# Kernel tuning notes

Hardware: AMD Instinct MI355X
Metric: run time of the kernel (lower is better)

## Reference

```python
import jax, jax.numpy as jnp
import numpy as np

B, I, H, D, PF, K = 256, 1024, 8, 128, 2, 4
P = PF * I          # up-projection width
HD = H * D          # hidden dim
EPS = 1e-5


def setup_inputs() -> dict:
    key = jax.random.key(0)
    ks = jax.random.split(key, 16)
    g = lambda k, shape, s=0.02: (jax.random.normal(k, shape, jnp.float32) * s)
    return dict(
        seq=jax.random.normal(ks[0], (B, I), jnp.float32),
        c0=jnp.zeros((B, H, D, D), jnp.float32),
        n0=jnp.ones((B, H, D), jnp.float32),
        m0=jnp.zeros((B, H), jnp.float32),
        ln_g=jnp.ones((I,), jnp.float32), ln_b=jnp.zeros((I,), jnp.float32),
        gn_g=jnp.ones((HD,), jnp.float32), gn_b=jnp.zeros((HD,), jnp.float32),
        W_upl=g(ks[1], (P, I)), b_upl=jnp.zeros((P,), jnp.float32),
        W_upr=g(ks[2], (HD, I)), b_upr=jnp.zeros((HD,), jnp.float32),
        W_down=g(ks[3], (I, HD)), b_down=jnp.zeros((I,), jnp.float32),
        conv_w=g(ks[4], (K,), 0.3), conv_b=jnp.zeros((1,), jnp.float32),
        W_skip=g(ks[5], (HD, P)),
        W_i=g(ks[6], (H, P)), b_i=jnp.zeros((H,), jnp.float32),
        W_f=g(ks[7], (H, P)), b_f=jnp.zeros((H,), jnp.float32),
        W_o=g(ks[8], (HD, P)), b_o=jnp.zeros((HD,), jnp.float32),
        W_q=g(ks[9], (HD, P)), b_q=jnp.zeros((HD,), jnp.float32),
        W_k=g(ks[10], (HD, P)), b_k=jnp.zeros((HD,), jnp.float32),
        W_v=g(ks[11], (HD, P)), b_v=jnp.zeros((HD,), jnp.float32),
    )


def reference(seq, c0, n0, m0, ln_g, ln_b, gn_g, gn_b,
              W_upl, b_upl, W_upr, b_upr, W_down, b_down,
              conv_w, conv_b, W_skip,
              W_i, b_i, W_f, b_f, W_o, b_o,
              W_q, b_q, W_k, b_k, W_v, b_v):
    # LayerNorm on input
    mu = seq.mean(-1, keepdims=True)
    var = seq.var(-1, keepdims=True)
    x_n = (seq - mu) / jnp.sqrt(var + EPS) * ln_g + ln_b

    x_t = x_n @ W_upl.T + b_upl      # [B, P]
    r_t = x_n @ W_upr.T + b_upr      # [B, HD]

    # Causal conv (kernel K) along the feature axis of x_t
    xp = jnp.pad(x_t, ((0, 0), (K - 1, 0)))
    x_c = sum(conv_w[j] * xp[:, j:j + P] for j in range(K)) + conv_b[0]
    x_c = jax.nn.silu(x_c)           # [B, P]

    q = (x_c @ W_q.T + b_q).reshape(B, H, D)
    k = (x_c @ W_k.T + b_k).reshape(B, H, D) / np.float32(np.sqrt(D))
    v = (x_t @ W_v.T + b_v).reshape(B, H, D)

    i_t = x_c @ W_i.T + b_i          # [B, H]
    f_t = x_c @ W_f.T + b_f          # [B, H]
    o_t = jax.nn.sigmoid(x_t @ W_o.T + b_o)  # [B, HD]

    # Stabilized exponential gating
    m_t = jnp.maximum(f_t + m0, i_t)
    i_e = jnp.exp(i_t - m_t)
    f_e = jnp.exp(f_t - m_t + m0)

    # Matrix-memory covariance update: f*C + i*(v x k)
    c_t = f_e[:, :, None, None] * c0 + i_e[:, :, None, None] * jnp.einsum('bhd,bhp->bhdp', v, k)
    n_t = f_e[:, :, None] * n0 + i_e[:, :, None] * k

    num = jnp.einsum('bhdp,bhp->bhd', c_t, q)
    den = jnp.clip(jnp.einsum('bhd,bhd->bh', n_t, q), 1.0, None)[..., None]
    h_t = o_t * (num / den).reshape(B, HD)

    # GroupNorm: H groups of D channels, per-channel affine
    hg = h_t.reshape(B, H, D)
    gmu = hg.mean(-1, keepdims=True)
    gvar = hg.var(-1, keepdims=True)
    h_norm = ((hg - gmu) / jnp.sqrt(gvar + EPS)).reshape(B, HD) * gn_g + gn_b

    out = h_norm + x_c @ W_skip.T    # skip: 1x1 conv == linear, no bias
    out = out * jax.nn.silu(r_t)
    out = out @ W_down.T + b_down
    return (out + seq, c_t, n_t, m_t)
```

## Files before the change

kernel.cpp:

```cpp
#include <hip/hip_runtime.h>
#include <hip/hip_bf16.h>

typedef __attribute__((ext_vector_type(8))) short short8;
typedef __attribute__((ext_vector_type(4))) float f32x4;

__device__ __forceinline__ unsigned short f2bf(float x) {
  union { float f; unsigned int u; } v; v.f = x;
  unsigned int r = v.u + 0x7FFFu + ((v.u >> 16) & 1u);
  return (unsigned short)(r >> 16);
}

__global__ __launch_bounds__(256) void ln_kernel(
    const float* __restrict__ seq, const float* __restrict__ g,
    const float* __restrict__ b, unsigned short* __restrict__ xnb) {
  int row = blockIdx.x;
  int tid = threadIdx.x;
  const float* x = seq + (size_t)row * 1024;
  float4 v = *(const float4*)(x + tid * 4);
  float s = v.x + v.y + v.z + v.w;
  float s2 = v.x * v.x + v.y * v.y + v.z * v.z + v.w * v.w;
#pragma unroll
  for (int off = 32; off; off >>= 1) { s += __shfl_down(s, off); s2 += __shfl_down(s2, off); }
  __shared__ float rs_[4], rs2_[4];
  int lane = tid & 63, wave = tid >> 6;
  if (lane == 0) { rs_[wave] = s; rs2_[wave] = s2; }
  __syncthreads();
  float sum = rs_[0] + rs_[1] + rs_[2] + rs_[3];
  float sum2 = rs2_[0] + rs2_[1] + rs2_[2] + rs2_[3];
  float mu = sum * (1.f / 1024.f);
  float var = sum2 * (1.f / 1024.f) - mu * mu;
  float rstd = rsqrtf(var + 1e-5f);
  float4 gg = *(const float4*)(g + tid * 4);
  float4 bb = *(const float4*)(b + tid * 4);
  ushort4 o;
  o.x = f2bf((v.x - mu) * rstd * gg.x + bb.x);
  o.y = f2bf((v.y - mu) * rstd * gg.y + bb.y);
  o.z = f2bf((v.z - mu) * rstd * gg.z + bb.z);
  o.w = f2bf((v.w - mu) * rstd * gg.w + bb.w);
  *(ushort4*)(xnb + (size_t)row * 1024 + tid * 4) = o;
}

struct GemmSegs {
  const unsigned short* A[8];
  const float* W[8];
  const float* bias[8];
  const float* add[8];
  float* out[8];
  int N[8];
  int tile0[8];
  int act[8];
  float scale[8];
  int nseg;
  int K;
};

#define SB 72

__global__ __launch_bounds__(256, 4) void gemm_multi(GemmSegs g) {
  __shared__ __align__(16) unsigned short As[64 * SB];
  __shared__ __align__(16) unsigned short Ws[64 * SB];
  int bid = blockIdx.x;
  int m0 = (bid & 3) * 64;
  int tIdx = bid >> 2;
  int s = 0;
  while (s + 1 < g.nseg && tIdx >= g.tile0[s + 1]) s++;
  int n0 = (tIdx - g.tile0[s]) * 64;
  const unsigned short* A = g.A[s];
  const float* W = g.W[s];
  int N = g.N[s], Kd = g.K;
  int tid = threadIdx.x;
  int lane = tid & 63, wave = tid >> 6, quad = lane >> 4, l16 = lane & 15;

  f32x4 acc[4] = {};

  int r_ = tid >> 2;
  int c_ = (tid & 3) * 16;

  const unsigned short* aRow = A + (size_t)(m0 + r_) * Kd + c_;
  const float* wRow = W + (size_t)(n0 + r_) * Kd + c_;
  bool wOk = (n0 + r_) < N;

  uint4 a0 = *(const uint4*)(aRow);
  uint4 a1 = *(const uint4*)(aRow + 8);
  float4 w0 = make_float4(0, 0, 0, 0), w1 = w0, w2 = w0, w3 = w0;
  if (wOk) {
    w0 = *(const float4*)(wRow);
    w1 = *(const float4*)(wRow + 4);
    w2 = *(const float4*)(wRow + 8);
    w3 = *(const float4*)(wRow + 12);
  }

  for (int k0 = 0; k0 < Kd; k0 += 64) {
    *(uint4*)&As[r_ * SB + c_] = a0;
    *(uint4*)&As[r_ * SB + c_ + 8] = a1;
    uint4 u0, u1;
    u0.x = (unsigned)f2bf(w0.x) | ((unsigned)f2bf(w0.y) << 16);
    u0.y = (unsigned)f2bf(w0.z) | ((unsigned)f2bf(w0.w) << 16);
    u0.z = (unsigned)f2bf(w1.x) | ((unsigned)f2bf(w1.y) << 16);
    u0.w = (unsigned)f2bf(w1.z) | ((unsigned)f2bf(w1.w) << 16);
    u1.x = (unsigned)f2bf(w2.x) | ((unsigned)f2bf(w2.y) << 16);
    u1.y = (unsigned)f2bf(w2.z) | ((unsigned)f2bf(w2.w) << 16);
    u1.z = (unsigned)f2bf(w3.x) | ((unsigned)f2bf(w3.y) << 16);
    u1.w = (unsigned)f2bf(w3.z) | ((unsigned)f2bf(w3.w) << 16);
    *(uint4*)&Ws[r_ * SB + c_] = u0;
    *(uint4*)&Ws[r_ * SB + c_ + 8] = u1;
    __syncthreads();
    if (k0 + 64 < Kd) {
      a0 = *(const uint4*)(aRow + k0 + 64);
      a1 = *(const uint4*)(aRow + k0 + 72);
      if (wOk) {
        w0 = *(const float4*)(wRow + k0 + 64);
        w1 = *(const float4*)(wRow + k0 + 68);
        w2 = *(const float4*)(wRow + k0 + 72);
        w3 = *(const float4*)(wRow + k0 + 76);
      }
    }
#pragma unroll
    for (int kc = 0; kc < 2; kc++) {
      int kb = kc * 32 + quad * 8;
      short8 af = *(const short8*)&As[(wave * 16 + l16) * SB + kb];
#pragma unroll
      for (int c = 0; c < 4; c++) {
        short8 bfr = *(const short8*)&Ws[(c * 16 + l16) * SB + kb];
        acc[c] = __builtin_amdgcn_mfma_f32_16x16x32_bf16(af, bfr, acc[c], 0, 0, 0);
      }
    }
    __syncthreads();
  }

  const float* bias = g.bias[s];
  const float* add = g.add[s];
  float* out = g.out[s];
  int act = g.act[s];
  float scale = g.scale[s];
#pragma unroll
  for (int c = 0; c < 4; c++) {
    int n = n0 + c * 16 + l16;
    if (n >= N) continue;
    float bv = bias ? bias[n] : 0.f;
#pragma unroll
    for (int j = 0; j < 4; j++) {
      int m = m0 + wave * 16 + quad * 4 + j;
      float val = acc[c][j] + bv;
      if (act == 1) val = val / (1.f + __expf(-val));
      else if (act == 2) val = 1.f / (1.f + __expf(-val));
      val *= scale;
      size_t idx = (size_t)m * N + n;
      if (act == 3) val += add[idx];
      out[idx] = val;
    }
  }
}

__global__ __launch_bounds__(256) void conv_kernel(
    const float* __restrict__ xt, const float* __restrict__ conv_w,
    const float* __restrict__ conv_b, unsigned short* __restrict__ xcb,
    unsigned short* __restrict__ xtb) {
  int b = blockIdx.x;
  int tid = threadIdx.x;
  __shared__ float xr[2048];
  const float* row = xt + (size_t)b * 2048;
#pragma unroll
  for (int it = 0; it < 2; it++) {
    int i = (it * 256 + tid) * 4;
    *(float4*)&xr[i] = *(const float4*)(row + i);
  }
  __syncthreads();
  float w0 = conv_w[0], w1 = conv_w[1], w2 = conv_w[2], w3 = conv_w[3], cb = conv_b[0];
#pragma unroll
  for (int it = 0; it < 2; it++) {
    int i0 = (it * 256 + tid) * 4;
    ushort4 oc, ot;
    unsigned short* pc = &oc.x;
    unsigned short* pt = &ot.x;
#pragma unroll
    for (int j = 0; j < 4; j++) {
      int i = i0 + j;
      float x3 = xr[i];
      float x2 = (i >= 1) ? xr[i - 1] : 0.f;
      float x1 = (i >= 2) ? xr[i - 2] : 0.f;
      float x0 = (i >= 3) ? xr[i - 3] : 0.f;
      float c = w0 * x0 + w1 * x1 + w2 * x2 + w3 * x3 + cb;
      c = c / (1.f + __expf(-c));
      pc[j] = f2bf(c);
      pt[j] = f2bf(x3);
    }
    *(ushort4*)(xcb + (size_t)b * 2048 + i0) = oc;
    *(ushort4*)(xtb + (size_t)b * 2048 + i0) = ot;
  }
}

__global__ __launch_bounds__(256) void cell_kernel(
    const float* __restrict__ c0, const float* __restrict__ n0,
    const float* __restrict__ m0, const float* __restrict__ qb,
    const float* __restrict__ kb, const float* __restrict__ vb,
    const float* __restrict__ ob, const float* __restrict__ skipb,
    const float* __restrict__ srb, const float* __restrict__ itb,
    const float* __restrict__ ftb, const float* __restrict__ gn_g,
    const float* __restrict__ gn_b, float* __restrict__ ct_out,
    float* __restrict__ nt_out, float* __restrict__ mt_out,
    unsigned short* __restrict__ yb) {
  int bh = blockIdx.x;
  int h = bh & 7;
  int tid = threadIdx.x;
  int lane = tid & 63, wave = tid >> 6;
  __shared__ float qs[128], ks[128], vs[128], num[128];
  __shared__ float r0[4], r1[4];

  float i_t = itb[bh], f_t = ftb[bh], m0v = m0[bh];
  float m_t = fmaxf(f_t + m0v, i_t);
  float i_e = __expf(i_t - m_t);
  float f_e = __expf(f_t - m_t + m0v);
  if (tid == 0) mt_out[bh] = m_t;

  size_t vbase = (size_t)bh * 128;
  float kq_p = 0.f, nq_p = 0.f, n0d = 0.f, kd = 0.f;
  if (tid < 128) {
    float qd = qb[vbase + tid];
    kd = kb[vbase + tid];
    n0d = n0[vbase + tid];
    qs[tid] = qd; ks[tid] = kd; vs[tid] = vb[vbase + tid];
    kq_p = kd * qd;
    nq_p = n0d * qd;
  }
#pragma unroll
  for (int off = 32; off; off >>= 1) { kq_p += __shfl_down(kq_p, off); nq_p += __shfl_down(nq_p, off); }
  if (lane == 0) { r0[wave] = kq_p; r1[wave] = nq_p; }
  __syncthreads();
  float kq = r0[0] + r0[1] + r0[2] + r0[3];
  float nq = r1[0] + r1[1] + r1[2] + r1[3];
  float den = fmaxf(f_e * nq + i_e * kq, 1.f);

  if (tid < 128) nt_out[vbase + tid] = f_e * n0d + i_e * kd;

  int rsub = lane >> 3;
  int cblk = lane & 7;
  int ccol = cblk * 16;
  float kr[16], qr[16];
#pragma unroll
  for (int j = 0; j < 16; j += 4) {
    *(float4*)&kr[j] = *(const float4*)&ks[ccol + j];
    *(float4*)&qr[j] = *(const float4*)&qs[ccol + j];
  }
  const float* c0p = c0 + (size_t)bh * 16384;
  float* ctp = ct_out + (size_t)bh * 16384;
#pragma unroll
  for (int gI = 0; gI < 4; gI++) {
    int d = wave * 32 + gI * 8 + rsub;
    float iv = i_e * vs[d];
    const float* src = c0p + d * 128 + ccol;
    float* dst = ctp + d * 128 + ccol;
    float p = 0.f;
#pragma unroll
    for (int j = 0; j < 4; j++) {
      float4 cv = *(const float4*)(src + j * 4);
      float4 cn;
      cn.x = f_e * cv.x + iv * kr[j * 4 + 0];
      cn.y = f_e * cv.y + iv * kr[j * 4 + 1];
      cn.z = f_e * cv.z + iv * kr[j * 4 + 2];
      cn.w = f_e * cv.w + iv * kr[j * 4 + 3];
      *(float4*)(dst + j * 4) = cn;
      p += cn.x * qr[j * 4 + 0] + cn.y * qr[j * 4 + 1] +
           cn.z * qr[j * 4 + 2] + cn.w * qr[j * 4 + 3];
    }
    p += __shfl_xor(p, 1);
    p += __shfl_xor(p, 2);
    p += __shfl_xor(p, 4);
    if (cblk == 0) num[d] = p;
  }
  __syncthreads();

  float hval = 0.f;
  if (tid < 128) hval = ob[vbase + tid] * num[tid] / den;
  float s = hval, s2 = hval * hval;
#pragma unroll
  for (int off = 32; off; off >>= 1) { s += __shfl_down(s, off); s2 += __shfl_down(s2, off); }
  if (lane == 0) { r0[wave] = s; r1[wave] = s2; }
  __syncthreads();
  float mean = (r0[0] + r0[1] + r0[2] + r0[3]) * (1.f / 128.f);
  float var = (r1[0] + r1[1] + r1[2] + r1[3]) * (1.f / 128.f) - mean * mean;
  float rstd = rsqrtf(var + 1e-5f);
  if (tid < 128) {
    int ch = h * 128 + tid;
    float hn = (hval - mean) * rstd * gn_g[ch] + gn_b[ch];
    float y = (hn + skipb[vbase + tid]) * srb[vbase + tid];
    yb[vbase + tid] = f2bf(y);
  }
}

extern "C" void kernel_launch(void* const* d_in, const int* in_sizes, int n_in,
                              void* d_out, int out_size, void* d_ws, size_t ws_size,
                              hipStream_t stream) {
  const float* seq   = (const float*)d_in[0];
  const float* c0    = (const float*)d_in[1];
  const float* n0    = (const float*)d_in[2];
  const float* m0    = (const float*)d_in[3];
  const float* ln_g  = (const float*)d_in[4];
  const float* ln_b  = (const float*)d_in[5];
  const float* gn_g  = (const float*)d_in[6];
  const float* gn_b  = (const float*)d_in[7];
  const float* W_upl = (const float*)d_in[8];
  const float* b_upl = (const float*)d_in[9];
  const float* W_upr = (const float*)d_in[10];
  const float* b_upr = (const float*)d_in[11];
  const float* W_down= (const float*)d_in[12];
  const float* b_down= (const float*)d_in[13];
  const float* conv_w= (const float*)d_in[14];
  const float* conv_b= (const float*)d_in[15];
  const float* W_skip= (const float*)d_in[16];
  const float* W_i   = (const float*)d_in[17];
  const float* b_i   = (const float*)d_in[18];
  const float* W_f   = (const float*)d_in[19];
  const float* b_f   = (const float*)d_in[20];
  const float* W_o   = (const float*)d_in[21];
  const float* b_o   = (const float*)d_in[22];
  const float* W_q   = (const float*)d_in[23];
  const float* b_q   = (const float*)d_in[24];
  const float* W_k   = (const float*)d_in[25];
  const float* b_k   = (const float*)d_in[26];
  const float* W_v   = (const float*)d_in[27];
  const float* b_v   = (const float*)d_in[28];

  float* out = (float*)d_out;
  float* ct  = out + 262144;
  float* nt  = ct + 33554432;
  float* mt  = nt + 262144;

  char* ws = (char*)d_ws;
  unsigned short* xnb = (unsigned short*)(ws);
  unsigned short* xtb = (unsigned short*)(ws + 524288);
  unsigned short* xcb = (unsigned short*)(ws + 1572864);
  unsigned short* yb  = (unsigned short*)(ws + 2621440);
  float* xt  = (float*)(ws + 3145728);
  float* sr  = (float*)(ws + 5242880);
  float* qb  = (float*)(ws + 6291456);
  float* kb  = (float*)(ws + 7340032);
  float* vb  = (float*)(ws + 8388608);
  float* ob  = (float*)(ws + 9437184);
  float* skb = (float*)(ws + 10485760);
  float* itb = (float*)(ws + 11534336);
  float* ftb = (float*)(ws + 11542528);

  ln_kernel<<<256, 256, 0, stream>>>(seq, ln_g, ln_b, xnb);

  GemmSegs g1 = {};
  g1.nseg = 2; g1.K = 1024;
  g1.A[0] = xnb; g1.W[0] = W_upl; g1.bias[0] = b_upl; g1.out[0] = xt;
  g1.N[0] = 2048; g1.tile0[0] = 0;  g1.act[0] = 0; g1.scale[0] = 1.f;
  g1.A[1] = xnb; g1.W[1] = W_upr; g1.bias[1] = b_upr; g1.out[1] = sr;
  g1.N[1] = 1024; g1.tile0[1] = 32; g1.act[1] = 1; g1.scale[1] = 1.f;
  gemm_multi<<<48 * 4, 256, 0, stream>>>(g1);

  conv_kernel<<<256, 256, 0, stream>>>(xt, conv_w, conv_b, xcb, xtb);

  GemmSegs g2 = {};
  g2.nseg = 7; g2.K = 2048;
  g2.A[0] = xcb; g2.W[0] = W_q;    g2.bias[0] = b_q;    g2.out[0] = qb;
  g2.N[0] = 1024; g2.tile0[0] = 0;  g2.act[0] = 0; g2.scale[0] = 1.f;
  g2.A[1] = xcb; g2.W[1] = W_k;    g2.bias[1] = b_k;    g2.out[1] = kb;
  g2.N[1] = 1024; g2.tile0[1] = 16; g2.act[1] = 0; g2.scale[1] = 0.088388347648318447f;
  g2.A[2] = xtb; g2.W[2] = W_v;    g2.bias[2] = b_v;    g2.out[2] = vb;
  g2.N[2] = 1024; g2.tile0[2] = 32; g2.act[2] = 0; g2.scale[2] = 1.f;
  g2.A[3] = xtb; g2.W[3] = W_o;    g2.bias[3] = b_o;    g2.out[3] = ob;
  g2.N[3] = 1024; g2.tile0[3] = 48; g2.act[3] = 2; g2.scale[3] = 1.f;
  g2.A[4] = xcb; g2.W[4] = W_skip; g2.bias[4] = nullptr; g2.out[4] = skb;
  g2.N[4] = 1024; g2.tile0[4] = 64; g2.act[4] = 0; g2.scale[4] = 1.f;
  g2.A[5] = xcb; g2.W[5] = W_i;    g2.bias[5] = b_i;    g2.out[5] = itb;
  g2.N[5] = 8;    g2.tile0[5] = 80; g2.act[5] = 0; g2.scale[5] = 1.f;
  g2.A[6] = xcb; g2.W[6] = W_f;    g2.bias[6] = b_f;    g2.out[6] = ftb;
  g2.N[6] = 8;    g2.tile0[6] = 81; g2.act[6] = 0; g2.scale[6] = 1.f;
  gemm_multi<<<82 * 4, 256, 0, stream>>>(g2);

  cell_kernel<<<2048, 256, 0, stream>>>(c0, n0, m0, qb, kb, vb, ob, skb, sr,
                                        itb, ftb, gn_g, gn_b, ct, nt, mt, yb);

  GemmSegs g3 = {};
  g3.nseg = 1; g3.K = 1024;
  g3.A[0] = yb; g3.W[0] = W_down; g3.bias[0] = b_down; g3.add[0] = seq; g3.out[0] = out;
  g3.N[0] = 1024; g3.tile0[0] = 0; g3.act[0] = 3; g3.scale[0] = 1.f;
  gemm_multi<<<16 * 4, 256, 0, stream>>>(g3);
}
```

Before: 419.1 us.

## Pre-convert weights to bf16 in a prep kernel and coalesce cell C-update

A new prep_kernel converts all fp32 weight matrices to bf16 once per call into workspace. The GEMMs then load bf16 weights directly, removing the per-tile fp32 load and bf16 conversion that was repeated across the four M-blocks. This adds an extra launch and a full pass over the weights (fp32 read, bf16 write). Separately, the cell kernel's C-state update now has 32 lanes cover each 128-float row with float4 accesses over 16 passes, for more coalesced memory traffic, at the cost of a longer shuffle reduction per row.

```diff
diff --git a/kernel.cpp b/kernel.cpp
--- a/kernel.cpp
+++ b/kernel.cpp
@@ -8,6 +8,35 @@
   union { float f; unsigned int u; } v; v.f = x;
   unsigned int r = v.u + 0x7FFFu + ((v.u >> 16) & 1u);
   return (unsigned short)(r >> 16);
+}
+
+struct PrepSegs {
+  const float* src[10];
+  unsigned short* dst[10];
+  int blk0[10];
+  int nseg;
+};
+
+__global__ __launch_bounds__(256) void prep_kernel(PrepSegs p) {
+  int bid = blockIdx.x;
+  int s = 0;
+  while (s + 1 < p.nseg && bid >= p.blk0[s + 1]) s++;
+  size_t off = (size_t)(bid - p.blk0[s]) * 8192;
+  const float* src = p.src[s] + off;
+  unsigned short* dst = p.dst[s] + off;
+  int tid = threadIdx.x;
+#pragma unroll
+  for (int j = 0; j < 4; j++) {
+    int i = (j * 256 + tid) * 8;
+    float4 a = *(const float4*)(src + i);
+    float4 b = *(const float4*)(src + i + 4);
+    uint4 o;
+    o.x = (unsigned)f2bf(a.x) | ((unsigned)f2bf(a.y) << 16);
+    o.y = (unsigned)f2bf(a.z) | ((unsigned)f2bf(a.w) << 16);
+    o.z = (unsigned)f2bf(b.x) | ((unsigned)f2bf(b.y) << 16);
+    o.w = (unsigned)f2bf(b.z) | ((unsigned)f2bf(b.w) << 16);
+    *(uint4*)(dst + i) = o;
+  }
 }
 
 __global__ __launch_bounds__(256) void ln_kernel(
@@ -42,7 +71,7 @@
 
 struct GemmSegs {
   const unsigned short* A[8];
-  const float* W[8];
+  const unsigned short* W[8];
   const float* bias[8];
   const float* add[8];
   float* out[8];
@@ -66,7 +95,7 @@
   while (s + 1 < g.nseg && tIdx >= g.tile0[s + 1]) s++;
   int n0 = (tIdx - g.tile0[s]) * 64;
   const unsigned short* A = g.A[s];
-  const float* W = g.W[s];
+  const unsigned short* W = g.W[s];
   int N = g.N[s], Kd = g.K;
   int tid = threadIdx.x;
   int lane = tid & 63, wave = tid >> 6, quad = lane >> 4, l16 = lane & 15;
@@ -77,42 +106,30 @@
   int c_ = (tid & 3) * 16;
 
   const unsigned short* aRow = A + (size_t)(m0 + r_) * Kd + c_;
-  const float* wRow = W + (size_t)(n0 + r_) * Kd + c_;
+  const unsigned short* wRow = W + (size_t)(n0 + r_) * Kd + c_;
   bool wOk = (n0 + r_) < N;
 
+  uint4 zz = make_uint4(0, 0, 0, 0);
   uint4 a0 = *(const uint4*)(aRow);
   uint4 a1 = *(const uint4*)(aRow + 8);
-  float4 w0 = make_float4(0, 0, 0, 0), w1 = w0, w2 = w0, w3 = w0;
+  uint4 w0 = zz, w1 = zz;
   if (wOk) {
-    w0 = *(const float4*)(wRow);
-    w1 = *(const float4*)(wRow + 4);
-    w2 = *(const float4*)(wRow + 8);
-    w3 = *(const float4*)(wRow + 12);
+    w0 = *(const uint4*)(wRow);
+    w1 = *(const uint4*)(wRow + 8);
   }
 
   for (int k0 = 0; k0 < Kd; k0 += 64) {
     *(uint4*)&As[r_ * SB + c_] = a0;
     *(uint4*)&As[r_ * SB + c_ + 8] = a1;
-    uint4 u0, u1;
-    u0.x = (unsigned)f2bf(w0.x) | ((unsigned)f2bf(w0.y) << 16);
-    u0.y = (unsigned)f2bf(w0.z) | ((unsigned)f2bf(w0.w) << 16);
-    u0.z = (unsigned)f2bf(w1.x) | ((unsigned)f2bf(w1.y) << 16);
-    u0.w = (unsigned)f2bf(w1.z) | ((unsigned)f2bf(w1.w) << 16);
-    u1.x = (unsigned)f2bf(w2.x) | ((unsigned)f2bf(w2.y) << 16);
-    u1.y = (unsigned)f2bf(w2.z) | ((unsigned)f2bf(w2.w) << 16);
-    u1.z = (unsigned)f2bf(w3.x) | ((unsigned)f2bf(w3.y) << 16);
-    u1.w = (unsigned)f2bf(w3.z) | ((unsigned)f2bf(w3.w) << 16);
-    *(uint4*)&Ws[r_ * SB + c_] = u0;
-    *(uint4*)&Ws[r_ * SB + c_ + 8] = u1;
+    *(uint4*)&Ws[r_ * SB + c_] = w0;
+    *(uint4*)&Ws[r_ * SB + c_ + 8] = w1;
     __syncthreads();
     if (k0 + 64 < Kd) {
       a0 = *(const uint4*)(aRow + k0 + 64);
       a1 = *(const uint4*)(aRow + k0 + 72);
       if (wOk) {
-        w0 = *(const float4*)(wRow + k0 + 64);
-        w1 = *(const float4*)(wRow + k0 + 68);
-        w2 = *(const float4*)(wRow + k0 + 72);
-        w3 = *(const float4*)(wRow + k0 + 76);
+        w0 = *(const uint4*)(wRow + k0 + 64);
+        w1 = *(const uint4*)(wRow + k0 + 72);
       }
     }
 #pragma unroll
@@ -233,40 +250,30 @@
 
   if (tid < 128) nt_out[vbase + tid] = f_e * n0d + i_e * kd;
 
-  int rsub = lane >> 3;
-  int cblk = lane & 7;
-  int ccol = cblk * 16;
-  float kr[16], qr[16];
-#pragma unroll
-  for (int j = 0; j < 16; j += 4) {
-    *(float4*)&kr[j] = *(const float4*)&ks[ccol + j];
-    *(float4*)&qr[j] = *(const float4*)&qs[ccol + j];
-  }
+  int col = (tid & 31) * 4;
+  int drow = tid >> 5;
+  float4 kr = *(const float4*)&ks[col];
+  float4 qr = *(const float4*)&qs[col];
   const float* c0p = c0 + (size_t)bh * 16384;
   float* ctp = ct_out + (size_t)bh * 16384;
-#pragma unroll
-  for (int gI = 0; gI < 4; gI++) {
-    int d = wave * 32 + gI * 8 + rsub;
+#pragma unroll 4
+  for (int pass = 0; pass < 16; pass++) {
+    int d = pass * 8 + drow;
     float iv = i_e * vs[d];
-    const float* src = c0p + d * 128 + ccol;
-    float* dst = ctp + d * 128 + ccol;
-    float p = 0.f;
-#pragma unroll
-    for (int j = 0; j < 4; j++) {
-      float4 cv = *(const float4*)(src + j * 4);
-      float4 cn;
-      cn.x = f_e * cv.x + iv * kr[j * 4 + 0];
-      cn.y = f_e * cv.y + iv * kr[j * 4 + 1];
-      cn.z = f_e * cv.z + iv * kr[j * 4 + 2];
-      cn.w = f_e * cv.w + iv * kr[j * 4 + 3];
-      *(float4*)(dst + j * 4) = cn;
-      p += cn.x * qr[j * 4 + 0] + cn.y * qr[j * 4 + 1] +
-           cn.z * qr[j * 4 + 2] + cn.w * qr[j * 4 + 3];
-    }
+    float4 cv = *(const float4*)(c0p + d * 128 + col);
+    float4 cn;
+    cn.x = f_e * cv.x + iv * kr.x;
+    cn.y = f_e * cv.y + iv * kr.y;
+    cn.z = f_e * cv.z + iv * kr.z;
+    cn.w = f_e * cv.w + iv * kr.w;
+    *(float4*)(ctp + d * 128 + col) = cn;
+    float p = cn.x * qr.x + cn.y * qr.y + cn.z * qr.z + cn.w * qr.w;
     p += __shfl_xor(p, 1);
     p += __shfl_xor(p, 2);
     p += __shfl_xor(p, 4);
-    if (cblk == 0) num[d] = p;
+    p += __shfl_xor(p, 8);
+    p += __shfl_xor(p, 16);
+    if ((tid & 31) == 0) num[d] = p;
   }
   __syncthreads();
 
@@ -340,14 +347,39 @@
   float* skb = (float*)(ws + 10485760);
   float* itb = (float*)(ws + 11534336);
   float* ftb = (float*)(ws + 11542528);
+  unsigned short* wb = (unsigned short*)(ws + 11550720);
+  unsigned short* wupl_b = wb;
+  unsigned short* wupr_b = wupl_b + 2097152;
+  unsigned short* wdown_b= wupr_b + 1048576;
+  unsigned short* wskip_b= wdown_b + 1048576;
+  unsigned short* wq_b   = wskip_b + 2097152;
+  unsigned short* wk_b   = wq_b + 2097152;
+  unsigned short* wv_b   = wk_b + 2097152;
+  unsigned short* wo_b   = wv_b + 2097152;
+  unsigned short* wi_b   = wo_b + 2097152;
+  unsigned short* wf_b   = wi_b + 16384;
+
+  PrepSegs pp = {};
+  pp.nseg = 10;
+  pp.src[0] = W_upl;  pp.dst[0] = wupl_b;  pp.blk0[0] = 0;
+  pp.src[1] = W_upr;  pp.dst[1] = wupr_b;  pp.blk0[1] = 256;
+  pp.src[2] = W_down; pp.dst[2] = wdown_b; pp.blk0[2] = 384;
+  pp.src[3] = W_skip; pp.dst[3] = wskip_b; pp.blk0[3] = 512;
+  pp.src[4] = W_q;    pp.dst[4] = wq_b;    pp.blk0[4] = 768;
+  pp.src[5] = W_k;    pp.dst[5] = wk_b;    pp.blk0[5] = 1024;
+  pp.src[6] = W_v;    pp.dst[6] = wv_b;    pp.blk0[6] = 1280;
+  pp.src[7] = W_o;    pp.dst[7] = wo_b;    pp.blk0[7] = 1536;
+  pp.src[8] = W_i;    pp.dst[8] = wi_b;    pp.blk0[8] = 1792;
+  pp.src[9] = W_f;    pp.dst[9] = wf_b;    pp.blk0[9] = 1794;
+  prep_kernel<<<1796, 256, 0, stream>>>(pp);
 
   ln_kernel<<<256, 256, 0, stream>>>(seq, ln_g, ln_b, xnb);
 
   GemmSegs g1 = {};
   g1.nseg = 2; g1.K = 1024;
-  g1.A[0] = xnb; g1.W[0] = W_upl; g1.bias[0] = b_upl; g1.out[0] = xt;
+  g1.A[0] = xnb; g1.W[0] = wupl_b; g1.bias[0] = b_upl; g1.out[0] = xt;
   g1.N[0] = 2048; g1.tile0[0] = 0;  g1.act[0] = 0; g1.scale[0] = 1.f;
-  g1.A[1] = xnb; g1.W[1] = W_upr; g1.bias[1] = b_upr; g1.out[1] = sr;
+  g1.A[1] = xnb; g1.W[1] = wupr_b; g1.bias[1] = b_upr; g1.out[1] = sr;
   g1.N[1] = 1024; g1.tile0[1] = 32; g1.act[1] = 1; g1.scale[1] = 1.f;
   gemm_multi<<<48 * 4, 256, 0, stream>>>(g1);
 
@@ -355,19 +387,19 @@
 
   GemmSegs g2 = {};
   g2.nseg = 7; g2.K = 2048;
-  g2.A[0] = xcb; g2.W[0] = W_q;    g2.bias[0] = b_q;    g2.out[0] = qb;
+  g2.A[0] = xcb; g2.W[0] = wq_b;    g2.bias[0] = b_q;    g2.out[0] = qb;
   g2.N[0] = 1024; g2.tile0[0] = 0;  g2.act[0] = 0; g2.scale[0] = 1.f;
-  g2.A[1] = xcb; g2.W[1] = W_k;    g2.bias[1] = b_k;    g2.out[1] = kb;
+  g2.A[1] = xcb; g2.W[1] = wk_b;    g2.bias[1] = b_k;    g2.out[1] = kb;
   g2.N[1] = 1024; g2.tile0[1] = 16; g2.act[1] = 0; g2.scale[1] = 0.088388347648318447f;
-  g2.A[2] = xtb; g2.W[2] = W_v;    g2.bias[2] = b_v;    g2.out[2] = vb;
+  g2.A[2] = xtb; g2.W[2] = wv_b;    g2.bias[2] = b_v;    g2.out[2] = vb;
   g2.N[2] = 1024; g2.tile0[2] = 32; g2.act[2] = 0; g2.scale[2] = 1.f;
-  g2.A[3] = xtb; g2.W[3] = W_o;    g2.bias[3] = b_o;    g2.out[3] = ob;
+  g2.A[3] = xtb; g2.W[3] = wo_b;    g2.bias[3] = b_o;    g2.out[3] = ob;
   g2.N[3] = 1024; g2.tile0[3] = 48; g2.act[3] = 2; g2.scale[3] = 1.f;
-  g2.A[4] = xcb; g2.W[4] = W_skip; g2.bias[4] = nullptr; g2.out[4] = skb;
+  g2.A[4] = xcb; g2.W[4] = wskip_b; g2.bias[4] = nullptr; g2.out[4] = skb;
   g2.N[4] = 1024; g2.tile0[4] = 64; g2.act[4] = 0; g2.scale[4] = 1.f;
-  g2.A[5] = xcb; g2.W[5] = W_i;    g2.bias[5] = b_i;    g2.out[5] = itb;
+  g2.A[5] = xcb; g2.W[5] = wi_b;    g2.bias[5] = b_i;    g2.out[5] = itb;
   g2.N[5] = 8;    g2.tile0[5] = 80; g2.act[5] = 0; g2.scale[5] = 1.f;
-  g2.A[6] = xcb; g2.W[6] = W_f;    g2.bias[6] = b_f;    g2.out[6] = ftb;
+  g2.A[6] = xcb; g2.W[6] = wf_b;    g2.bias[6] = b_f;    g2.out[6] = ftb;
   g2.N[6] = 8;    g2.tile0[6] = 81; g2.act[6] = 0; g2.scale[6] = 1.f;
   gemm_multi<<<82 * 4, 256, 0, stream>>>(g2);
 
@@ -376,7 +408,7 @@
 
   GemmSegs g3 = {};
   g3.nseg = 1; g3.K = 1024;
-  g3.A[0] = yb; g3.W[0] = W_down; g3.bias[0] = b_down; g3.add[0] = seq; g3.out[0] = out;
+  g3.A[0] = yb; g3.W[0] = wdown_b; g3.bias[0] = b_down; g3.add[0] = seq; g3.out[0] = out;
   g3.N[0] = 1024; g3.tile0[0] = 0; g3.act[0] = 3; g3.scale[0] = 1.f;
   gemm_multi<<<16 * 4, 256, 0, stream>>>(g3);
 }
```

Measured after the change: 398.4 us. -4.9%, faster.

## Halve GEMM M-tile, double-buffer LDS, and coalesce cell-kernel covariance update

Applied to the files above, without the earlier changes.

The GEMM M-tile shrinks from 64 to 32 rows, which doubles the grid so more blocks cover the CUs on these small-M matmuls. The four waves now sit in a 2x2 arrangement, each owning 16x32 of the output. The LDS tiles are double-buffered, so the next tile's stores happen after the MFMAs, which drops one barrier per k-step. The cell kernel now assigns 32 threads per row with float4 columns, so each row of c0/c_t is read and written contiguously across lanes, at the cost of a longer shuffle reduction. The trade-off is that weight tiles are reloaded and converted twice as often across the grid.

```diff
diff --git a/kernel.cpp b/kernel.cpp
--- a/kernel.cpp
+++ b/kernel.cpp
@@ -57,11 +57,11 @@
 #define SB 72
 
 __global__ __launch_bounds__(256, 4) void gemm_multi(GemmSegs g) {
-  __shared__ __align__(16) unsigned short As[64 * SB];
-  __shared__ __align__(16) unsigned short Ws[64 * SB];
+  __shared__ __align__(16) unsigned short As[2][32 * SB];
+  __shared__ __align__(16) unsigned short Ws[2][64 * SB];
   int bid = blockIdx.x;
-  int m0 = (bid & 3) * 64;
-  int tIdx = bid >> 2;
+  int m0 = (bid & 7) * 32;
+  int tIdx = bid >> 3;
   int s = 0;
   while (s + 1 < g.nseg && tIdx >= g.tile0[s + 1]) s++;
   int n0 = (tIdx - g.tile0[s]) * 64;
@@ -70,19 +70,20 @@
   int N = g.N[s], Kd = g.K;
   int tid = threadIdx.x;
   int lane = tid & 63, wave = tid >> 6, quad = lane >> 4, l16 = lane & 15;
-
-  f32x4 acc[4] = {};
-
-  int r_ = tid >> 2;
-  int c_ = (tid & 3) * 16;
-
-  const unsigned short* aRow = A + (size_t)(m0 + r_) * Kd + c_;
-  const float* wRow = W + (size_t)(n0 + r_) * Kd + c_;
-  bool wOk = (n0 + r_) < N;
-
+  int wm = wave & 1, wn = wave >> 1;
+
+  f32x4 acc[2] = {};
+
+  int ra = tid >> 3, ca = (tid & 7) * 8;
+  int rw = tid >> 2, cw = (tid & 3) * 16;
+
+  const unsigned short* aRow = A + (size_t)(m0 + ra) * Kd + ca;
+  const float* wRow = W + (size_t)(n0 + rw) * Kd + cw;
+  bool wOk = (n0 + rw) < N;
+
+  float4 z4 = make_float4(0.f, 0.f, 0.f, 0.f);
   uint4 a0 = *(const uint4*)(aRow);
-  uint4 a1 = *(const uint4*)(aRow + 8);
-  float4 w0 = make_float4(0, 0, 0, 0), w1 = w0, w2 = w0, w3 = w0;
+  float4 w0 = z4, w1 = z4, w2 = z4, w3 = z4;
   if (wOk) {
     w0 = *(const float4*)(wRow);
     w1 = *(const float4*)(wRow + 4);
@@ -90,9 +91,8 @@
     w3 = *(const float4*)(wRow + 12);
   }
 
-  for (int k0 = 0; k0 < Kd; k0 += 64) {
-    *(uint4*)&As[r_ * SB + c_] = a0;
-    *(uint4*)&As[r_ * SB + c_ + 8] = a1;
+  {
+    *(uint4*)&As[0][ra * SB + ca] = a0;
     uint4 u0, u1;
     u0.x = (unsigned)f2bf(w0.x) | ((unsigned)f2bf(w0.y) << 16);
     u0.y = (unsigned)f2bf(w0.z) | ((unsigned)f2bf(w0.w) << 16);
@@ -102,12 +102,16 @@
     u1.y = (unsigned)f2bf(w2.z) | ((unsigned)f2bf(w2.w) << 16);
     u1.z = (unsigned)f2bf(w3.x) | ((unsigned)f2bf(w3.y) << 16);
     u1.w = (unsigned)f2bf(w3.z) | ((unsigned)f2bf(w3.w) << 16);
-    *(uint4*)&Ws[r_ * SB + c_] = u0;
-    *(uint4*)&Ws[r_ * SB + c_ + 8] = u1;
+    *(uint4*)&Ws[0][rw * SB + cw] = u0;
+    *(uint4*)&Ws[0][rw * SB + cw + 8] = u1;
+  }
+
+  int buf = 0;
+  for (int k0 = 0; k0 < Kd; k0 += 64) {
     __syncthreads();
-    if (k0 + 64 < Kd) {
+    bool more = (k0 + 64) < Kd;
+    if (more) {
       a0 = *(const uint4*)(aRow + k0 + 64);
-      a1 = *(const uint4*)(aRow + k0 + 72);
       if (wOk) {
         w0 = *(const float4*)(wRow + k0 + 64);
         w1 = *(const float4*)(wRow + k0 + 68);
@@ -118,14 +122,29 @@
 #pragma unroll
     for (int kc = 0; kc < 2; kc++) {
       int kb = kc * 32 + quad * 8;
-      short8 af = *(const short8*)&As[(wave * 16 + l16) * SB + kb];
-#pragma unroll
-      for (int c = 0; c < 4; c++) {
-        short8 bfr = *(const short8*)&Ws[(c * 16 + l16) * SB + kb];
+      short8 af = *(const short8*)&As[buf][(wm * 16 + l16) * SB + kb];
+#pragma unroll
+      for (int c = 0; c < 2; c++) {
+        short8 bfr = *(const short8*)&Ws[buf][(wn * 32 + c * 16 + l16) * SB + kb];
         acc[c] = __builtin_amdgcn_mfma_f32_16x16x32_bf16(af, bfr, acc[c], 0, 0, 0);
       }
     }
-    __syncthreads();
+    if (more) {
+      int nb = buf ^ 1;
+      *(uint4*)&As[nb][ra * SB + ca] = a0;
+      uint4 u0, u1;
+      u0.x = (unsigned)f2bf(w0.x) | ((unsigned)f2bf(w0.y) << 16);
+      u0.y = (unsigned)f2bf(w0.z) | ((unsigned)f2bf(w0.w) << 16);
+      u0.z = (unsigned)f2bf(w1.x) | ((unsigned)f2bf(w1.y) << 16);
+      u0.w = (unsigned)f2bf(w1.z) | ((unsigned)f2bf(w1.w) << 16);
+      u1.x = (unsigned)f2bf(w2.x) | ((unsigned)f2bf(w2.y) << 16);
+      u1.y = (unsigned)f2bf(w2.z) | ((unsigned)f2bf(w2.w) << 16);
+      u1.z = (unsigned)f2bf(w3.x) | ((unsigned)f2bf(w3.y) << 16);
+      u1.w = (unsigned)f2bf(w3.z) | ((unsigned)f2bf(w3.w) << 16);
+      *(uint4*)&Ws[nb][rw * SB + cw] = u0;
+      *(uint4*)&Ws[nb][rw * SB + cw + 8] = u1;
+    }
+    buf ^= 1;
   }
 
   const float* bias = g.bias[s];
@@ -134,13 +153,13 @@
   int act = g.act[s];
   float scale = g.scale[s];
 #pragma unroll
-  for (int c = 0; c < 4; c++) {
-    int n = n0 + c * 16 + l16;
+  for (int c = 0; c < 2; c++) {
+    int n = n0 + wn * 32 + c * 16 + l16;
     if (n >= N) continue;
     float bv = bias ? bias[n] : 0.f;
 #pragma unroll
     for (int j = 0; j < 4; j++) {
-      int m = m0 + wave * 16 + quad * 4 + j;
+      int m = m0 + wm * 16 + quad * 4 + j;
       float val = acc[c][j] + bv;
       if (act == 1) val = val / (1.f + __expf(-val));
       else if (act == 2) val = 1.f / (1.f + __expf(-val));
@@ -233,40 +252,30 @@
 
   if (tid < 128) nt_out[vbase + tid] = f_e * n0d + i_e * kd;
 
-  int rsub = lane >> 3;
-  int cblk = lane & 7;
-  int ccol = cblk * 16;
-  float kr[16], qr[16];
-#pragma unroll
-  for (int j = 0; j < 16; j += 4) {
-    *(float4*)&kr[j] = *(const float4*)&ks[ccol + j];
-    *(float4*)&qr[j] = *(const float4*)&qs[ccol + j];
-  }
+  int col = (tid & 31) * 4;
+  int drow = tid >> 5;
+  float4 kr = *(const float4*)&ks[col];
+  float4 qr = *(const float4*)&qs[col];
   const float* c0p = c0 + (size_t)bh * 16384;
   float* ctp = ct_out + (size_t)bh * 16384;
-#pragma unroll
-  for (int gI = 0; gI < 4; gI++) {
-    int d = wave * 32 + gI * 8 + rsub;
+#pragma unroll 4
+  for (int pass = 0; pass < 16; pass++) {
+    int d = pass * 8 + drow;
     float iv = i_e * vs[d];
-    const float* src = c0p + d * 128 + ccol;
-    float* dst = ctp + d * 128 + ccol;
-    float p = 0.f;
-#pragma unroll
-    for (int j = 0; j < 4; j++) {
-      float4 cv = *(const float4*)(src + j * 4);
-      float4 cn;
-      cn.x = f_e * cv.x + iv * kr[j * 4 + 0];
-      cn.y = f_e * cv.y + iv * kr[j * 4 + 1];
-      cn.z = f_e * cv.z + iv * kr[j * 4 + 2];
-      cn.w = f_e * cv.w + iv * kr[j * 4 + 3];
-      *(float4*)(dst + j * 4) = cn;
-      p += cn.x * qr[j * 4 + 0] + cn.y * qr[j * 4 + 1] +
-           cn.z * qr[j * 4 + 2] + cn.w * qr[j * 4 + 3];
-    }
+    float4 cv = *(const float4*)(c0p + d * 128 + col);
+    float4 cn;
+    cn.x = f_e * cv.x + iv * kr.x;
+    cn.y = f_e * cv.y + iv * kr.y;
+    cn.z = f_e * cv.z + iv * kr.z;
+    cn.w = f_e * cv.w + iv * kr.w;
+    *(float4*)(ctp + d * 128 + col) = cn;
+    float p = cn.x * qr.x + cn.y * qr.y + cn.z * qr.z + cn.w * qr.w;
     p += __shfl_xor(p, 1);
     p += __shfl_xor(p, 2);
     p += __shfl_xor(p, 4);
-    if (cblk == 0) num[d] = p;
+    p += __shfl_xor(p, 8);
+    p += __shfl_xor(p, 16);
+    if ((tid & 31) == 0) num[d] = p;
   }
   __syncthreads();
 
@@ -349,7 +358,7 @@
   g1.N[0] = 2048; g1.tile0[0] = 0;  g1.act[0] = 0; g1.scale[0] = 1.f;
   g1.A[1] = xnb; g1.W[1] = W_upr; g1.bias[1] = b_upr; g1.out[1] = sr;
   g1.N[1] = 1024; g1.tile0[1] = 32; g1.act[1] = 1; g1.scale[1] = 1.f;
-  gemm_multi<<<48 * 4, 256, 0, stream>>>(g1);
+  gemm_multi<<<48 * 8, 256, 0, stream>>>(g1);
 
   conv_kernel<<<256, 256, 0, stream>>>(xt, conv_w, conv_b, xcb, xtb);
 
@@ -369,7 +378,7 @@
   g2.N[5] = 8;    g2.tile0[5] = 80; g2.act[5] = 0; g2.scale[5] = 1.f;
   g2.A[6] = xcb; g2.W[6] = W_f;    g2.bias[6] = b_f;    g2.out[6] = ftb;
   g2.N[6] = 8;    g2.tile0[6] = 81; g2.act[6] = 0; g2.scale[6] = 1.f;
-  gemm_multi<<<82 * 4, 256, 0, stream>>>(g2);
+  gemm_multi<<<82 * 8, 256, 0, stream>>>(g2);
 
   cell_kernel<<<2048, 256, 0, stream>>>(c0, n0, m0, qb, kb, vb, ob, skb, sr,
                                         itb, ftb, gn_g, gn_b, ct, nt, mt, yb);
@@ -378,5 +387,5 @@
   g3.nseg = 1; g3.K = 1024;
   g3.A[0] = yb; g3.W[0] = W_down; g3.bias[0] = b_down; g3.add[0] = seq; g3.out[0] = out;
   g3.N[0] = 1024; g3.tile0[0] = 0; g3.act[0] = 3; g3.scale[0] = 1.f;
-  gemm_multi<<<16 * 4, 256, 0, stream>>>(g3);
-}
+  gemm_multi<<<16 * 8, 256, 0, stream>>>(g3);
+}
```

Result: no change. 417.0 us (-0.5%).
